# Optimization experiments

Measured on AMD Instinct MI355X. Metric: run time of the kernel, lower is better.

The kernel has to match this reference:

```python
import jax, jax.numpy as jnp
import numpy as np

N = 50000
E = 800000
F_IN = 128
HID = 128
NCLS = 64


def setup_inputs() -> dict:
    key = jax.random.key(0)
    ks = jax.random.split(key, 10)
    x = jax.random.normal(ks[0], (N, F_IN), dtype=jnp.float32)
    edge_index = jax.random.randint(ks[1], (2, E), 0, N, dtype=jnp.int64)
    def w(k, fi, fo):
        return jax.random.normal(k, (fi, fo), dtype=jnp.float32) / np.sqrt(fi)
    return {
        "x": x,
        "edge_index": edge_index,
        "W1": w(ks[2], F_IN, HID), "b1": jnp.zeros((HID,), jnp.float32),
        "W2": w(ks[3], HID, HID), "b2": jnp.zeros((HID,), jnp.float32),
        "W3": w(ks[4], HID, HID), "b3": jnp.zeros((HID,), jnp.float32),
        "W4": w(ks[5], HID, NCLS), "b4": jnp.zeros((NCLS,), jnp.float32),
    }


def _build_graph(edge_index, n):
    # PyG GCNConv default: add self loops, symmetric normalization D^-1/2 (A+I) D^-1/2
    loops = jnp.arange(n, dtype=edge_index.dtype)
    row = jnp.concatenate([edge_index[0], loops])  # source
    col = jnp.concatenate([edge_index[1], loops])  # destination
    deg = jax.ops.segment_sum(jnp.ones_like(col, dtype=jnp.float32), col, num_segments=n)
    dinv = jnp.where(deg > 0, jax.lax.rsqrt(deg), 0.0)
    norm = dinv[row] * dinv[col]  # [E+N]
    return row, col, norm


def _gcn_layer(x, row, col, norm, W, b, n):
    h = x @ W                                    # [N, out]
    msg = h[row] * norm[:, None]                 # gather + scale, [E+N, out]
    out = jax.ops.segment_sum(msg, col, num_segments=n)  # scatter-add
    return out + b


def reference(x, edge_index, W1, b1, W2, b2, W3, b3, W4, b4):
    n = x.shape[0]
    row, col, norm = _build_graph(edge_index, n)
    h = jax.nn.relu(_gcn_layer(x, row, col, norm, W1, b1, n))
    h = jax.nn.relu(_gcn_layer(h, row, col, norm, W2, b2, n))
    h = jax.nn.relu(_gcn_layer(h, row, col, norm, W3, b3, n))
    return _gcn_layer(h, row, col, norm, W4, b4, n)
```

## Files before the change

### kernel.cpp

```cpp
#include <hip/hip_runtime.h>
#include <hip/hip_fp16.h>
#include <type_traits>

#define N_NODES 50000
#define N_EDGES 800000
#define WIN_BITS 9
#define WIN 512
#define NBUK ((N_NODES + WIN - 1) / WIN)
#define BCAP 16384

typedef _Float16 half8 __attribute__((ext_vector_type(8)));
typedef float floatx4 __attribute__((ext_vector_type(4)));

__global__ __launch_bounds__(256) void p0_bucket(const int* __restrict__ ei,
                                                 int* __restrict__ gcur,
                                                 unsigned* __restrict__ arena, int E) {
    __shared__ int lcnt[NBUK];
    __shared__ int lbase[NBUK];
    int tid = threadIdx.x;
    int chunk = (E + gridDim.x - 1) / gridDim.x;
    int e0 = blockIdx.x * chunk;
    int e1 = e0 + chunk; if (e1 > E) e1 = E;
    for (int b = tid; b < NBUK; b += 256) lcnt[b] = 0;
    __syncthreads();
    for (int e = e0 + tid; e < e1; e += 256) {
        int dst = ei[E + e];
        atomicAdd(&lcnt[dst >> WIN_BITS], 1);
    }
    __syncthreads();
    for (int b = tid; b < NBUK; b += 256) {
        lbase[b] = atomicAdd(&gcur[b], lcnt[b]);
        lcnt[b] = 0;
    }
    __syncthreads();
    for (int e = e0 + tid; e < e1; e += 256) {
        int dst = ei[E + e];
        int src = ei[e];
        int b = dst >> WIN_BITS;
        int pos = lbase[b] + atomicAdd(&lcnt[b], 1);
        if (pos < BCAP)
            arena[(size_t)b * BCAP + pos] = ((unsigned)src << WIN_BITS) | (unsigned)(dst & (WIN - 1));
    }
}

__global__ void scan_buckets(const int* __restrict__ gcur, int* __restrict__ bukoff,
                             int* __restrict__ offsets, int n, int total) {
    __shared__ int s[128];
    int t = threadIdx.x;
    int v = (t < NBUK) ? gcur[t] : 0;
    s[t] = v;
    __syncthreads();
    for (int off = 1; off < 128; off <<= 1) {
        int u = (t >= off) ? s[t - off] : 0;
        __syncthreads();
        s[t] += u;
        __syncthreads();
    }
    if (t < NBUK) bukoff[t] = s[t] - v;
    if (t == 0) offsets[n] = total;
}

__global__ __launch_bounds__(256) void p1_count_scan(const unsigned* __restrict__ arena,
                                                     const int* __restrict__ gcur,
                                                     const int* __restrict__ bukoff,
                                                     int* __restrict__ offsets,
                                                     float* __restrict__ dinv, int n) {
    __shared__ int cnt[WIN];
    __shared__ int sbuf[256];
    int b = blockIdx.x, tid = threadIdx.x;
    cnt[tid] = 0; cnt[tid + 256] = 0;
    __syncthreads();
    int m = gcur[b]; if (m > BCAP) m = BCAP;
    const unsigned* a = arena + (size_t)b * BCAP;
    for (int i = tid; i < m; i += 256) atomicAdd(&cnt[a[i] & (WIN - 1)], 1);
    __syncthreads();
    int j0 = tid * 2;
    int a0 = cnt[j0], a1 = cnt[j0 + 1];
    int ts = a0 + a1;
    sbuf[tid] = ts;
    __syncthreads();
    for (int off = 1; off < 256; off <<= 1) {
        int u = (tid >= off) ? sbuf[tid - off] : 0;
        __syncthreads();
        sbuf[tid] += u;
        __syncthreads();
    }
    int pre = sbuf[tid] - ts;
    int base = b << WIN_BITS;
    int o0 = bukoff[b] + pre, o1 = o0 + a0;
    int d0 = base + j0;
    if (d0 + 1 < n) {
        *(int2*)&offsets[d0] = make_int2(o0, o1);
        *(float2*)&dinv[d0] = make_float2(rsqrtf((float)(a0 + 1)), rsqrtf((float)(a1 + 1)));
    } else if (d0 < n) {
        offsets[d0] = o0;
        dinv[d0] = rsqrtf((float)(a0 + 1));
    }
}

__global__ __launch_bounds__(256) void p2_fill(const unsigned* __restrict__ arena,
                                               const int* __restrict__ gcur,
                                               const int* __restrict__ offsets,
                                               int* __restrict__ csr_src, int n) {
    __shared__ int cur[WIN];
    int b = blockIdx.x, tid = threadIdx.x;
    int base = b << WIN_BITS;
    for (int j = tid; j < WIN; j += 256) {
        int d = base + j;
        cur[j] = (d < n) ? offsets[d] : 0;
    }
    __syncthreads();
    int m = gcur[b]; if (m > BCAP) m = BCAP;
    const unsigned* a = arena + (size_t)b * BCAP;
    for (int i = tid; i < m; i += 256) {
        unsigned e = a[i];
        int pos = atomicAdd(&cur[e & (WIN - 1)], 1);
        csr_src[pos] = (int)(e >> WIN_BITS);
    }
}

__global__ void wfrag_kernel(const float* __restrict__ W, _Float16* __restrict__ Wf, int FO) {
    int g = blockIdx.x * 256 + threadIdx.x;
    if (g >= 16 * FO) return;
    int col = g % FO;
    int sq = g / FO;
    int k0 = sq * 8;
    half8 hv;
    #pragma unroll
    for (int j = 0; j < 8; ++j)
        hv[j] = (_Float16)W[(size_t)(k0 + j) * FO + col];
    *(half8*)&Wf[(size_t)g * 8] = hv;
}

template<int FO, typename InT>
__global__ __launch_bounds__(256) void gemm_mfma_kernel(
        const InT* __restrict__ x, const float* __restrict__ W,
        const float* __restrict__ dinv, __half* __restrict__ h, int n) {
    constexpr int NT = FO / 16;
    __shared__ _Float16 wlds[16 * FO * 8];

    int tid = threadIdx.x;
    constexpr int G = 16 * FO;
    for (int it = 0; it < G / 256; ++it) {
        int g = tid + it * 256;
        int col = g % FO;
        int sq = g / FO;
        int k0 = sq * 8;
        half8 hv;
        #pragma unroll
        for (int j = 0; j < 8; ++j)
            hv[j] = (_Float16)W[(size_t)(k0 + j) * FO + col];
        *(half8*)&wlds[(size_t)g * 8] = hv;
    }
    __syncthreads();

    int ln = tid & 15;
    int q  = (tid >> 4) & 3;
    int w  = tid >> 6;
    int node = blockIdx.x * 64 + w * 16 + ln;
    int nodec = node < n ? node : n - 1;
    const InT* xrow = x + (size_t)nodec * 128;

    floatx4 acc[NT];
    #pragma unroll
    for (int t = 0; t < NT; ++t) acc[t] = (floatx4){0.f, 0.f, 0.f, 0.f};

    #pragma unroll
    for (int s = 0; s < 4; ++s) {
        half8 xf;
        if constexpr (std::is_same_v<InT, float>) {
            const float* xp = xrow + s * 32 + q * 8;
            float4 a0 = *(const float4*)xp;
            float4 a1 = *(const float4*)(xp + 4);
            xf[0] = (_Float16)a0.x; xf[1] = (_Float16)a0.y;
            xf[2] = (_Float16)a0.z; xf[3] = (_Float16)a0.w;
            xf[4] = (_Float16)a1.x; xf[5] = (_Float16)a1.y;
            xf[6] = (_Float16)a1.z; xf[7] = (_Float16)a1.w;
        } else {
            xf = *(const half8*)(xrow + s * 32 + q * 8);
        }
        int sq = s * 4 + q;
        #pragma unroll
        for (int t = 0; t < NT; ++t) {
            half8 wf = *(const half8*)&wlds[(size_t)(sq * FO + t * 16 + ln) * 8];
            acc[t] = __builtin_amdgcn_mfma_f32_16x16x32_f16(wf, xf, acc[t], 0, 0, 0);
        }
    }

    if (node < n) {
        float dv = dinv[node];
        __half* hrow = h + (size_t)node * FO;
        #pragma unroll
        for (int t = 0; t < NT; ++t) {
            __half2 p[2];
            p[0] = __float22half2_rn(make_float2(acc[t][0] * dv, acc[t][1] * dv));
            p[1] = __float22half2_rn(make_float2(acc[t][2] * dv, acc[t][3] * dv));
            *(uint2*)&hrow[t * 16 + q * 4] = *(const uint2*)p;
        }
    }
}

template<int FO>
__global__ __launch_bounds__(512) void fused_agg_gemm(
        const __half2* __restrict__ hin, const int* __restrict__ offsets,
        const int* __restrict__ csr_src, const float* __restrict__ dinv,
        const float* __restrict__ bias, const _Float16* __restrict__ Wfrag,
        __half* __restrict__ hout, int n) {
    constexpr int NT  = FO / 16;
    constexpr int TPW = NT / 2;
    __shared__ _Float16 aggL[64 * 136];

    int tid = threadIdx.x;

    int w = tid >> 6;
    int lane = tid & 63;
    float2 bb = ((const float2*)bias)[lane];
    __half2* aggRow = (__half2*)aggL;
    for (int ii = 0; ii < 8; ++ii) {
        int c = blockIdx.x * 64 + w * 8 + ii;
        if (c >= n) break;
        c = __builtin_amdgcn_readfirstlane(c);
        float2 acc = __half22float2(hin[(size_t)c * 64 + lane]);
        int s = offsets[c], e = offsets[c + 1];
        int i = s;
        for (; i + 7 < e; i += 8) {
            int s0 = csr_src[i],     s1 = csr_src[i + 1], s2 = csr_src[i + 2], s3 = csr_src[i + 3];
            int s4 = csr_src[i + 4], s5 = csr_src[i + 5], s6 = csr_src[i + 6], s7 = csr_src[i + 7];
            float2 f0 = __half22float2(hin[(size_t)s0 * 64 + lane]);
            float2 f1 = __half22float2(hin[(size_t)s1 * 64 + lane]);
            float2 f2 = __half22float2(hin[(size_t)s2 * 64 + lane]);
            float2 f3 = __half22float2(hin[(size_t)s3 * 64 + lane]);
            float2 f4 = __half22float2(hin[(size_t)s4 * 64 + lane]);
            float2 f5 = __half22float2(hin[(size_t)s5 * 64 + lane]);
            float2 f6 = __half22float2(hin[(size_t)s6 * 64 + lane]);
            float2 f7 = __half22float2(hin[(size_t)s7 * 64 + lane]);
            acc.x += (f0.x + f1.x) + (f2.x + f3.x) + (f4.x + f5.x) + (f6.x + f7.x);
            acc.y += (f0.y + f1.y) + (f2.y + f3.y) + (f4.y + f5.y) + (f6.y + f7.y);
        }
        for (; i + 3 < e; i += 4) {
            int s0 = csr_src[i], s1 = csr_src[i + 1], s2 = csr_src[i + 2], s3 = csr_src[i + 3];
            float2 f0 = __half22float2(hin[(size_t)s0 * 64 + lane]);
            float2 f1 = __half22float2(hin[(size_t)s1 * 64 + lane]);
            float2 f2 = __half22float2(hin[(size_t)s2 * 64 + lane]);
            float2 f3 = __half22float2(hin[(size_t)s3 * 64 + lane]);
            acc.x += (f0.x + f1.x) + (f2.x + f3.x);
            acc.y += (f0.y + f1.y) + (f2.y + f3.y);
        }
        for (; i < e; ++i) {
            float2 f = __half22float2(hin[(size_t)csr_src[i] * 64 + lane]);
            acc.x += f.x; acc.y += f.y;
        }
        float dc = dinv[c];
        float vx = fmaxf(fmaf(acc.x, dc, bb.x), 0.0f);
        float vy = fmaxf(fmaf(acc.y, dc, bb.y), 0.0f);
        aggRow[(size_t)(w * 8 + ii) * 68 + lane] = __float22half2_rn(make_float2(vx, vy));
    }
    __syncthreads();

    int ng = w & 3, cg = w >> 2;
    int ln = tid & 15;
    int q  = (tid >> 4) & 3;
    int nl = ng * 16 + ln;
    int node = blockIdx.x * 64 + nl;

    floatx4 acc[TPW];
    #pragma unroll
    for (int t = 0; t < TPW; ++t) acc[t] = (floatx4){0.f, 0.f, 0.f, 0.f};

    #pragma unroll
    for (int s = 0; s < 4; ++s) {
        half8 xf = *(const half8*)&aggL[(size_t)nl * 136 + s * 32 + q * 8];
        int sq = s * 4 + q;
        #pragma unroll
        for (int t = 0; t < TPW; ++t) {
            int T = cg * TPW + t;
            half8 wf = *(const half8*)&Wfrag[(size_t)(sq * FO + T * 16 + ln) * 8];
            acc[t] = __builtin_amdgcn_mfma_f32_16x16x32_f16(wf, xf, acc[t], 0, 0, 0);
        }
    }

    if (node < n) {
        float dv = dinv[node];
        __half* hrow = hout + (size_t)node * FO;
        #pragma unroll
        for (int t = 0; t < TPW; ++t) {
            int T = cg * TPW + t;
            __half2 p[2];
            p[0] = __float22half2_rn(make_float2(acc[t][0] * dv, acc[t][1] * dv));
            p[1] = __float22half2_rn(make_float2(acc[t][2] * dv, acc[t][3] * dv));
            *(uint2*)&hrow[T * 16 + q * 4] = *(const uint2*)p;
        }
    }
}

__global__ __launch_bounds__(256) void agg64_kernel(
        const __half2* __restrict__ h2, const int* __restrict__ offsets,
        const int* __restrict__ csr_src, const float* __restrict__ dinv,
        const float* __restrict__ bias, float* __restrict__ out, int n) {
    int lane = threadIdx.x & 63;
    int hf = lane >> 5, sl = lane & 31;
    int c = (blockIdx.x << 2) + (threadIdx.x >> 6);
    if (c >= n) return;
    c = __builtin_amdgcn_readfirstlane(c);
    float2 acc = make_float2(0.0f, 0.0f);
    if (hf == 0) acc = __half22float2(h2[(size_t)c * 32 + sl]);
    int s = offsets[c], e = offsets[c + 1];
    int i = s;
    for (; i + 3 < e; i += 4) {
        int sa = csr_src[i + hf];
        int sb = csr_src[i + 2 + hf];
        float2 fa = __half22float2(h2[(size_t)sa * 32 + sl]);
        float2 fb = __half22float2(h2[(size_t)sb * 32 + sl]);
        acc.x += fa.x + fb.x; acc.y += fa.y + fb.y;
    }
    for (; i + 1 < e; i += 2) {
        int sa = csr_src[i + hf];
        float2 fa = __half22float2(h2[(size_t)sa * 32 + sl]);
        acc.x += fa.x; acc.y += fa.y;
    }
    if (i < e && hf == 0) {
        float2 fa = __half22float2(h2[(size_t)csr_src[i] * 32 + sl]);
        acc.x += fa.x; acc.y += fa.y;
    }
    acc.x += __shfl_xor(acc.x, 32);
    acc.y += __shfl_xor(acc.y, 32);
    if (hf == 0) {
        float dc = dinv[c];
        float2 bb = ((const float2*)bias)[sl];
        float2 o;
        o.x = fmaf(acc.x, dc, bb.x);
        o.y = fmaf(acc.y, dc, bb.y);
        ((float2*)out)[(size_t)c * 32 + sl] = o;
    }
}


extern "C" void kernel_launch(void* const* d_in, const int* in_sizes, int n_in,
                              void* d_out, int out_size, void* d_ws, size_t ws_size,
                              hipStream_t stream) {
    const float* x  = (const float*)d_in[0];
    const int*   ei = (const int*)  d_in[1];
    const float* W1 = (const float*)d_in[2];
    const float* b1 = (const float*)d_in[3];
    const float* W2 = (const float*)d_in[4];
    const float* b2 = (const float*)d_in[5];
    const float* W3 = (const float*)d_in[6];
    const float* b3 = (const float*)d_in[7];
    const float* W4 = (const float*)d_in[8];
    const float* b4 = (const float*)d_in[9];

    const int N = N_NODES, E = N_EDGES;

    char* p = (char*)d_ws;
    auto carve = [&](size_t bytes) {
        char* q = p;
        p += (bytes + 255) & ~(size_t)255;
        return (void*)q;
    };
    int*       offsets = (int*)      carve((size_t)(N + 1) * 4);
    int*       csr_src = (int*)      carve((size_t)E * 4);
    float*     dinv    = (float*)    carve((size_t)N * 4);
    int*       gcur    = (int*)      carve((size_t)NBUK * 4);
    int*       bukoff  = (int*)      carve((size_t)NBUK * 4);
    unsigned*  arena   = (unsigned*) carve((size_t)NBUK * BCAP * 4);
    _Float16*  Wf2     = (_Float16*) carve((size_t)16 * 128 * 8 * 2);
    _Float16*  Wf3     = (_Float16*) carve((size_t)16 * 128 * 8 * 2);
    _Float16*  Wf4     = (_Float16*) carve((size_t)16 * 64 * 8 * 2);
    __half*    A1      = (__half*)   carve((size_t)N * 128 * 2);
    __half*    A2      = (__half*)   carve((size_t)N * 128 * 2);

    hipMemsetAsync(gcur, 0, (size_t)NBUK * 4, stream);
    p0_bucket<<<512, 256, 0, stream>>>(ei, gcur, arena, E);
    scan_buckets<<<1, 128, 0, stream>>>(gcur, bukoff, offsets, N, E);
    p1_count_scan<<<NBUK, 256, 0, stream>>>(arena, gcur, bukoff, offsets, dinv, N);
    p2_fill<<<NBUK, 256, 0, stream>>>(arena, gcur, offsets, csr_src, N);
    wfrag_kernel<<<8, 256, 0, stream>>>(W2, Wf2, 128);
    wfrag_kernel<<<8, 256, 0, stream>>>(W3, Wf3, 128);
    wfrag_kernel<<<4, 256, 0, stream>>>(W4, Wf4, 64);

    const int nb64 = (N + 63) / 64;

    gemm_mfma_kernel<128, float><<<nb64, 256, 0, stream>>>(x, W1, dinv, A1, N);
    fused_agg_gemm<128><<<nb64, 512, 0, stream>>>((const __half2*)A1, offsets, csr_src, dinv, b1, Wf2, A2, N);
    fused_agg_gemm<128><<<nb64, 512, 0, stream>>>((const __half2*)A2, offsets, csr_src, dinv, b2, Wf3, A1, N);
    fused_agg_gemm<64><<<nb64, 512, 0, stream>>>((const __half2*)A1, offsets, csr_src, dinv, b3, Wf4, A2, N);
    agg64_kernel<<<(N + 3) / 4, 256, 0, stream>>>((const __half2*)A2, offsets, csr_src, dinv, b4, (float*)d_out, N);
}
```

Measured before the change: 285.1 us.

## Widen neighbor gathers to 16-byte loads and precompute all weight fragments

The aggregation loops in the fused layers and the final layer now have each lane load 8 halves (16 bytes) per neighbor row. Several neighbors are processed in parallel across lane groups and combined with cross-lane shuffles, instead of 4-byte per-lane loads of one neighbor at a time. The layer-1 GEMM now reads a precomputed fp16 weight fragment from global memory rather than converting W1 into shared memory in every block. The three weight-fragment launches are merged into one that also covers W1. The trade-off is more shuffle reductions, more registers per lane, and idle lane groups on low-degree tails.

```diff
diff --git a/kernel.cpp b/kernel.cpp
--- a/kernel.cpp
+++ b/kernel.cpp
@@ -11,6 +11,16 @@
 
 typedef _Float16 half8 __attribute__((ext_vector_type(8)));
 typedef float floatx4 __attribute__((ext_vector_type(4)));
+
+__device__ inline void acc8(float* a, half8 v) {
+    const __half2* p = (const __half2*)&v;
+    float2 f0 = __half22float2(p[0]);
+    float2 f1 = __half22float2(p[1]);
+    float2 f2 = __half22float2(p[2]);
+    float2 f3 = __half22float2(p[3]);
+    a[0] += f0.x; a[1] += f0.y; a[2] += f1.x; a[3] += f1.y;
+    a[4] += f2.x; a[5] += f2.y; a[6] += f3.x; a[7] += f3.y;
+}
 
 __global__ __launch_bounds__(256) void p0_bucket(const int* __restrict__ ei,
                                                  int* __restrict__ gcur,
@@ -119,8 +129,18 @@
     }
 }
 
-__global__ void wfrag_kernel(const float* __restrict__ W, _Float16* __restrict__ Wf, int FO) {
-    int g = blockIdx.x * 256 + threadIdx.x;
+__global__ __launch_bounds__(256) void wfrag_all(
+        const float* __restrict__ W1, const float* __restrict__ W2,
+        const float* __restrict__ W3, const float* __restrict__ W4,
+        _Float16* __restrict__ Wf1, _Float16* __restrict__ Wf2,
+        _Float16* __restrict__ Wf3, _Float16* __restrict__ Wf4) {
+    int b = blockIdx.x;
+    const float* W; _Float16* Wf; int FO; int lb;
+    if (b < 8)       { W = W1; Wf = Wf1; FO = 128; lb = b; }
+    else if (b < 16) { W = W2; Wf = Wf2; FO = 128; lb = b - 8; }
+    else if (b < 24) { W = W3; Wf = Wf3; FO = 128; lb = b - 16; }
+    else             { W = W4; Wf = Wf4; FO = 64;  lb = b - 24; }
+    int g = lb * 256 + threadIdx.x;
     if (g >= 16 * FO) return;
     int col = g % FO;
     int sq = g / FO;
@@ -132,34 +152,18 @@
     *(half8*)&Wf[(size_t)g * 8] = hv;
 }
 
-template<int FO, typename InT>
 __global__ __launch_bounds__(256) void gemm_mfma_kernel(
-        const InT* __restrict__ x, const float* __restrict__ W,
+        const float* __restrict__ x, const _Float16* __restrict__ Wfrag,
         const float* __restrict__ dinv, __half* __restrict__ h, int n) {
+    constexpr int FO = 128;
     constexpr int NT = FO / 16;
-    __shared__ _Float16 wlds[16 * FO * 8];
-
     int tid = threadIdx.x;
-    constexpr int G = 16 * FO;
-    for (int it = 0; it < G / 256; ++it) {
-        int g = tid + it * 256;
-        int col = g % FO;
-        int sq = g / FO;
-        int k0 = sq * 8;
-        half8 hv;
-        #pragma unroll
-        for (int j = 0; j < 8; ++j)
-            hv[j] = (_Float16)W[(size_t)(k0 + j) * FO + col];
-        *(half8*)&wlds[(size_t)g * 8] = hv;
-    }
-    __syncthreads();
-
     int ln = tid & 15;
     int q  = (tid >> 4) & 3;
     int w  = tid >> 6;
     int node = blockIdx.x * 64 + w * 16 + ln;
     int nodec = node < n ? node : n - 1;
-    const InT* xrow = x + (size_t)nodec * 128;
+    const float* xrow = x + (size_t)nodec * 128;
 
     floatx4 acc[NT];
     #pragma unroll
@@ -167,22 +171,18 @@
 
     #pragma unroll
     for (int s = 0; s < 4; ++s) {
+        const float* xp = xrow + s * 32 + q * 8;
+        float4 a0 = *(const float4*)xp;
+        float4 a1 = *(const float4*)(xp + 4);
         half8 xf;
-        if constexpr (std::is_same_v<InT, float>) {
-            const float* xp = xrow + s * 32 + q * 8;
-            float4 a0 = *(const float4*)xp;
-            float4 a1 = *(const float4*)(xp + 4);
-            xf[0] = (_Float16)a0.x; xf[1] = (_Float16)a0.y;
-            xf[2] = (_Float16)a0.z; xf[3] = (_Float16)a0.w;
-            xf[4] = (_Float16)a1.x; xf[5] = (_Float16)a1.y;
-            xf[6] = (_Float16)a1.z; xf[7] = (_Float16)a1.w;
-        } else {
-            xf = *(const half8*)(xrow + s * 32 + q * 8);
-        }
+        xf[0] = (_Float16)a0.x; xf[1] = (_Float16)a0.y;
+        xf[2] = (_Float16)a0.z; xf[3] = (_Float16)a0.w;
+        xf[4] = (_Float16)a1.x; xf[5] = (_Float16)a1.y;
+        xf[6] = (_Float16)a1.z; xf[7] = (_Float16)a1.w;
         int sq = s * 4 + q;
         #pragma unroll
         for (int t = 0; t < NT; ++t) {
-            half8 wf = *(const half8*)&wlds[(size_t)(sq * FO + t * 16 + ln) * 8];
+            half8 wf = *(const half8*)&Wfrag[(size_t)(sq * FO + t * 16 + ln) * 8];
             acc[t] = __builtin_amdgcn_mfma_f32_16x16x32_f16(wf, xf, acc[t], 0, 0, 0);
         }
     }
@@ -202,7 +202,7 @@
 
 template<int FO>
 __global__ __launch_bounds__(512) void fused_agg_gemm(
-        const __half2* __restrict__ hin, const int* __restrict__ offsets,
+        const _Float16* __restrict__ hin, const int* __restrict__ offsets,
         const int* __restrict__ csr_src, const float* __restrict__ dinv,
         const float* __restrict__ bias, const _Float16* __restrict__ Wfrag,
         __half* __restrict__ hout, int n) {
@@ -211,49 +211,59 @@
     __shared__ _Float16 aggL[64 * 136];
 
     int tid = threadIdx.x;
-
     int w = tid >> 6;
     int lane = tid & 63;
-    float2 bb = ((const float2*)bias)[lane];
-    __half2* aggRow = (__half2*)aggL;
+    int qw = lane >> 4, sl = lane & 15;
+    float4 bb0 = *(const float4*)&bias[sl * 8];
+    float4 bb1 = *(const float4*)&bias[sl * 8 + 4];
+
     for (int ii = 0; ii < 8; ++ii) {
         int c = blockIdx.x * 64 + w * 8 + ii;
         if (c >= n) break;
         c = __builtin_amdgcn_readfirstlane(c);
-        float2 acc = __half22float2(hin[(size_t)c * 64 + lane]);
+        float acc[8] = {0.f, 0.f, 0.f, 0.f, 0.f, 0.f, 0.f, 0.f};
+        if (qw == 0)
+            acc8(acc, *(const half8*)&hin[(size_t)c * 128 + sl * 8]);
         int s = offsets[c], e = offsets[c + 1];
         int i = s;
         for (; i + 7 < e; i += 8) {
-            int s0 = csr_src[i],     s1 = csr_src[i + 1], s2 = csr_src[i + 2], s3 = csr_src[i + 3];
-            int s4 = csr_src[i + 4], s5 = csr_src[i + 5], s6 = csr_src[i + 6], s7 = csr_src[i + 7];
-            float2 f0 = __half22float2(hin[(size_t)s0 * 64 + lane]);
-            float2 f1 = __half22float2(hin[(size_t)s1 * 64 + lane]);
-            float2 f2 = __half22float2(hin[(size_t)s2 * 64 + lane]);
-            float2 f3 = __half22float2(hin[(size_t)s3 * 64 + lane]);
-            float2 f4 = __half22float2(hin[(size_t)s4 * 64 + lane]);
-            float2 f5 = __half22float2(hin[(size_t)s5 * 64 + lane]);
-            float2 f6 = __half22float2(hin[(size_t)s6 * 64 + lane]);
-            float2 f7 = __half22float2(hin[(size_t)s7 * 64 + lane]);
-            acc.x += (f0.x + f1.x) + (f2.x + f3.x) + (f4.x + f5.x) + (f6.x + f7.x);
-            acc.y += (f0.y + f1.y) + (f2.y + f3.y) + (f4.y + f5.y) + (f6.y + f7.y);
+            int sa = csr_src[i + qw];
+            int sb = csr_src[i + 4 + qw];
+            half8 va = *(const half8*)&hin[(size_t)sa * 128 + sl * 8];
+            half8 vb = *(const half8*)&hin[(size_t)sb * 128 + sl * 8];
+            acc8(acc, va);
+            acc8(acc, vb);
         }
         for (; i + 3 < e; i += 4) {
-            int s0 = csr_src[i], s1 = csr_src[i + 1], s2 = csr_src[i + 2], s3 = csr_src[i + 3];
-            float2 f0 = __half22float2(hin[(size_t)s0 * 64 + lane]);
-            float2 f1 = __half22float2(hin[(size_t)s1 * 64 + lane]);
-            float2 f2 = __half22float2(hin[(size_t)s2 * 64 + lane]);
-            float2 f3 = __half22float2(hin[(size_t)s3 * 64 + lane]);
-            acc.x += (f0.x + f1.x) + (f2.x + f3.x);
-            acc.y += (f0.y + f1.y) + (f2.y + f3.y);
-        }
-        for (; i < e; ++i) {
-            float2 f = __half22float2(hin[(size_t)csr_src[i] * 64 + lane]);
-            acc.x += f.x; acc.y += f.y;
-        }
-        float dc = dinv[c];
-        float vx = fmaxf(fmaf(acc.x, dc, bb.x), 0.0f);
-        float vy = fmaxf(fmaf(acc.y, dc, bb.y), 0.0f);
-        aggRow[(size_t)(w * 8 + ii) * 68 + lane] = __float22half2_rn(make_float2(vx, vy));
+            int sa = csr_src[i + qw];
+            acc8(acc, *(const half8*)&hin[(size_t)sa * 128 + sl * 8]);
+        }
+        if (i + qw < e) {
+            int sa = csr_src[i + qw];
+            acc8(acc, *(const half8*)&hin[(size_t)sa * 128 + sl * 8]);
+        }
+        #pragma unroll
+        for (int k = 0; k < 8; ++k) {
+            acc[k] += __shfl_xor(acc[k], 16);
+            acc[k] += __shfl_xor(acc[k], 32);
+        }
+        if (qw == 0) {
+            float dc = dinv[c];
+            float v0 = fmaxf(fmaf(acc[0], dc, bb0.x), 0.f);
+            float v1 = fmaxf(fmaf(acc[1], dc, bb0.y), 0.f);
+            float v2 = fmaxf(fmaf(acc[2], dc, bb0.z), 0.f);
+            float v3 = fmaxf(fmaf(acc[3], dc, bb0.w), 0.f);
+            float v4 = fmaxf(fmaf(acc[4], dc, bb1.x), 0.f);
+            float v5 = fmaxf(fmaf(acc[5], dc, bb1.y), 0.f);
+            float v6 = fmaxf(fmaf(acc[6], dc, bb1.z), 0.f);
+            float v7 = fmaxf(fmaf(acc[7], dc, bb1.w), 0.f);
+            half8 hv;
+            hv[0] = (_Float16)v0; hv[1] = (_Float16)v1;
+            hv[2] = (_Float16)v2; hv[3] = (_Float16)v3;
+            hv[4] = (_Float16)v4; hv[5] = (_Float16)v5;
+            hv[6] = (_Float16)v6; hv[7] = (_Float16)v7;
+            *(half8*)&aggL[(size_t)(w * 8 + ii) * 136 + sl * 8] = hv;
+        }
     }
     __syncthreads();
 
@@ -294,43 +304,53 @@
 }
 
 __global__ __launch_bounds__(256) void agg64_kernel(
-        const __half2* __restrict__ h2, const int* __restrict__ offsets,
+        const _Float16* __restrict__ h, const int* __restrict__ offsets,
         const int* __restrict__ csr_src, const float* __restrict__ dinv,
         const float* __restrict__ bias, float* __restrict__ out, int n) {
     int lane = threadIdx.x & 63;
-    int hf = lane >> 5, sl = lane & 31;
+    int o = lane >> 3, sl = lane & 7;
     int c = (blockIdx.x << 2) + (threadIdx.x >> 6);
     if (c >= n) return;
     c = __builtin_amdgcn_readfirstlane(c);
-    float2 acc = make_float2(0.0f, 0.0f);
-    if (hf == 0) acc = __half22float2(h2[(size_t)c * 32 + sl]);
+    float acc[8] = {0.f, 0.f, 0.f, 0.f, 0.f, 0.f, 0.f, 0.f};
+    if (o == 0)
+        acc8(acc, *(const half8*)&h[(size_t)c * 64 + sl * 8]);
     int s = offsets[c], e = offsets[c + 1];
     int i = s;
-    for (; i + 3 < e; i += 4) {
-        int sa = csr_src[i + hf];
-        int sb = csr_src[i + 2 + hf];
-        float2 fa = __half22float2(h2[(size_t)sa * 32 + sl]);
-        float2 fb = __half22float2(h2[(size_t)sb * 32 + sl]);
-        acc.x += fa.x + fb.x; acc.y += fa.y + fb.y;
-    }
-    for (; i + 1 < e; i += 2) {
-        int sa = csr_src[i + hf];
-        float2 fa = __half22float2(h2[(size_t)sa * 32 + sl]);
-        acc.x += fa.x; acc.y += fa.y;
-    }
-    if (i < e && hf == 0) {
-        float2 fa = __half22float2(h2[(size_t)csr_src[i] * 32 + sl]);
-        acc.x += fa.x; acc.y += fa.y;
-    }
-    acc.x += __shfl_xor(acc.x, 32);
-    acc.y += __shfl_xor(acc.y, 32);
-    if (hf == 0) {
+    for (; i + 15 < e; i += 16) {
+        int sa = csr_src[i + o];
+        int sb = csr_src[i + 8 + o];
+        half8 va = *(const half8*)&h[(size_t)sa * 64 + sl * 8];
+        half8 vb = *(const half8*)&h[(size_t)sb * 64 + sl * 8];
+        acc8(acc, va);
+        acc8(acc, vb);
+    }
+    for (; i + 7 < e; i += 8) {
+        int sa = csr_src[i + o];
+        acc8(acc, *(const half8*)&h[(size_t)sa * 64 + sl * 8]);
+    }
+    if (i + o < e) {
+        int sa = csr_src[i + o];
+        acc8(acc, *(const half8*)&h[(size_t)sa * 64 + sl * 8]);
+    }
+    #pragma unroll
+    for (int k = 0; k < 8; ++k) {
+        acc[k] += __shfl_xor(acc[k], 8);
+        acc[k] += __shfl_xor(acc[k], 16);
+        acc[k] += __shfl_xor(acc[k], 32);
+    }
+    if (o == 0) {
         float dc = dinv[c];
-        float2 bb = ((const float2*)bias)[sl];
-        float2 o;
-        o.x = fmaf(acc.x, dc, bb.x);
-        o.y = fmaf(acc.y, dc, bb.y);
-        ((float2*)out)[(size_t)c * 32 + sl] = o;
+        float4 bb0 = *(const float4*)&bias[sl * 8];
+        float4 bb1 = *(const float4*)&bias[sl * 8 + 4];
+        float4 o0, o1;
+        o0.x = fmaf(acc[0], dc, bb0.x); o0.y = fmaf(acc[1], dc, bb0.y);
+        o0.z = fmaf(acc[2], dc, bb0.z); o0.w = fmaf(acc[3], dc, bb0.w);
+        o1.x = fmaf(acc[4], dc, bb1.x); o1.y = fmaf(acc[5], dc, bb1.y);
+        o1.z = fmaf(acc[6], dc, bb1.z); o1.w = fmaf(acc[7], dc, bb1.w);
+        float* orow = out + (size_t)c * 64 + sl * 8;
+        *(float4*)orow = o0;
+        *(float4*)(orow + 4) = o1;
     }
 }
 
@@ -363,6 +383,7 @@
     int*       gcur    = (int*)      carve((size_t)NBUK * 4);
     int*       bukoff  = (int*)      carve((size_t)NBUK * 4);
     unsigned*  arena   = (unsigned*) carve((size_t)NBUK * BCAP * 4);
+    _Float16*  Wf1     = (_Float16*) carve((size_t)16 * 128 * 8 * 2);
     _Float16*  Wf2     = (_Float16*) carve((size_t)16 * 128 * 8 * 2);
     _Float16*  Wf3     = (_Float16*) carve((size_t)16 * 128 * 8 * 2);
     _Float16*  Wf4     = (_Float16*) carve((size_t)16 * 64 * 8 * 2);
@@ -374,15 +395,13 @@
     scan_buckets<<<1, 128, 0, stream>>>(gcur, bukoff, offsets, N, E);
     p1_count_scan<<<NBUK, 256, 0, stream>>>(arena, gcur, bukoff, offsets, dinv, N);
     p2_fill<<<NBUK, 256, 0, stream>>>(arena, gcur, offsets, csr_src, N);
-    wfrag_kernel<<<8, 256, 0, stream>>>(W2, Wf2, 128);
-    wfrag_kernel<<<8, 256, 0, stream>>>(W3, Wf3, 128);
-    wfrag_kernel<<<4, 256, 0, stream>>>(W4, Wf4, 64);
+    wfrag_all<<<28, 256, 0, stream>>>(W1, W2, W3, W4, Wf1, Wf2, Wf3, Wf4);
 
     const int nb64 = (N + 63) / 64;
 
-    gemm_mfma_kernel<128, float><<<nb64, 256, 0, stream>>>(x, W1, dinv, A1, N);
-    fused_agg_gemm<128><<<nb64, 512, 0, stream>>>((const __half2*)A1, offsets, csr_src, dinv, b1, Wf2, A2, N);
-    fused_agg_gemm<128><<<nb64, 512, 0, stream>>>((const __half2*)A2, offsets, csr_src, dinv, b2, Wf3, A1, N);
-    fused_agg_gemm<64><<<nb64, 512, 0, stream>>>((const __half2*)A1, offsets, csr_src, dinv, b3, Wf4, A2, N);
-    agg64_kernel<<<(N + 3) / 4, 256, 0, stream>>>((const __half2*)A2, offsets, csr_src, dinv, b4, (float*)d_out, N);
-}
+    gemm_mfma_kernel<<<nb64, 256, 0, stream>>>(x, Wf1, dinv, A1, N);
+    fused_agg_gemm<128><<<nb64, 512, 0, stream>>>((const _Float16*)A1, offsets, csr_src, dinv, b1, Wf2, A2, N);
+    fused_agg_gemm<128><<<nb64, 512, 0, stream>>>((const _Float16*)A2, offsets, csr_src, dinv, b2, Wf3, A1, N);
+    fused_agg_gemm<64><<<nb64, 512, 0, stream>>>((const _Float16*)A1, offsets, csr_src, dinv, b3, Wf4, A2, N);
+    agg64_kernel<<<(N + 3) / 4, 256, 0, stream>>>((const _Float16*)A2, offsets, csr_src, dinv, b4, (float*)d_out, N);
+}
```

After: 280.8 us. About the same (-1.5%).
